# Kernel optimization log

Measured on AMD Instinct MI355X. Metric: run time of the kernel, lower is better.

## Reference

```python
import jax, jax.numpy as jnp
import numpy as np

N = 50000      # nodes
E = 1250000    # edges (avg degree 32)
D = 64         # in_channels == hidden_channels
L = 3          # num_layers
IMPROVED_FILL = 2.0  # GCNConv(improved=True) self-loop weight


def setup_inputs() -> dict:
    key = jax.random.key(0)
    ks = jax.random.split(key, 6)
    x = jax.random.normal(ks[0], (N, D), dtype=jnp.float32)
    edge_index = jax.random.randint(ks[1], (2, E), 0, N, dtype=jnp.int64)
    edge_weight = jax.random.uniform(ks[2], (E,), dtype=jnp.float32)
    Ws = jax.random.normal(ks[3], (L, D, D), dtype=jnp.float32) / np.sqrt(D).astype(np.float32)
    bs = jnp.zeros((L, D), dtype=jnp.float32)
    Wf = jax.random.normal(ks[4], (D, 1), dtype=jnp.float32) / np.sqrt(D).astype(np.float32)
    bf = jnp.zeros((1,), dtype=jnp.float32)
    return dict(x=x, edge_index=edge_index, edge_weight=edge_weight,
                Ws=Ws, bs=bs, Wf=Wf, bf=bf, prob=0)


def _gcn_norm(edge_index, edge_weight, n):
    # add self-loops with fill value 2.0 (improved=True)
    loop = jnp.arange(n, dtype=edge_index.dtype)
    row = jnp.concatenate([edge_index[0], loop])  # source nodes (x_j)
    col = jnp.concatenate([edge_index[1], loop])  # target nodes (aggregation)
    w = jnp.concatenate([edge_weight,
                         jnp.full((n,), IMPROVED_FILL, edge_weight.dtype)])
    deg = jax.ops.segment_sum(w, col, num_segments=n)
    dis = jnp.where(deg > 0, jax.lax.rsqrt(deg), 0.0)  # deg^{-1/2}, inf->0
    norm = dis[row] * w * dis[col]                      # [E+N]
    return row, col, norm


def reference(x, edge_index, edge_weight, Ws, bs, Wf, bf, prob):
    n = x.shape[0]
    # gcn_norm depends only on graph structure; compute once, reuse per layer
    row, col, norm = _gcn_norm(edge_index, edge_weight, n)
    for l in range(Ws.shape[0]):
        h = x @ Ws[l]                                  # [N, D] linear transform
        msg = h[row] * norm[:, None]                   # gather + per-edge scale
        agg = jax.ops.segment_sum(msg, col, num_segments=n)  # scatter-add
        x = jax.nn.relu(agg + bs[l])
    # F.dropout(x, p=prob) with prob=0 -> identity (inference)
    return x @ Wf + bf                                 # [N, 1]
```

## Files before the change

kernel.cpp:

```cpp
#include <hip/hip_runtime.h>
#include <hip/hip_bf16.h>

#define DCH 64
#define NB_CSR 256
#define MAXBINS 256

typedef __attribute__((ext_vector_type(8))) short bfrag;
typedef __attribute__((ext_vector_type(4))) float ffrag;

static __device__ __forceinline__ unsigned short f2bf(float f) {
    unsigned u = __float_as_uint(f);
    unsigned r = (u + 0x7fffu + ((u >> 16) & 1u)) >> 16;
    return (unsigned short)r;
}
static __device__ __forceinline__ float bf2f(unsigned short s) {
    return __uint_as_float(((unsigned)s) << 16);
}

__global__ __launch_bounds__(1024) void binc_k(const int* __restrict__ col,
                                               unsigned* __restrict__ blkcnt, int e) {
    __shared__ unsigned bins[MAXBINS];
    int B = blockIdx.x, tid = threadIdx.x;
    int chunk = (e + NB_CSR - 1) / NB_CSR;
    int beg = B * chunk, end = min(e, beg + chunk);
    if (tid < MAXBINS) bins[tid] = 0;
    __syncthreads();
    for (int i = beg + tid; i < end; i += 1024)
        atomicAdd(&bins[col[i] >> 8], 1u);
    __syncthreads();
    if (tid < MAXBINS) blkcnt[B * MAXBINS + tid] = bins[tid];
}

__global__ __launch_bounds__(64) void bincur1_k(const unsigned* __restrict__ blkcnt,
                                                unsigned* __restrict__ blkcur,
                                                unsigned* __restrict__ tot) {
    int j = blockIdx.x, lane = threadIdx.x;
    unsigned carry = 0;
#pragma unroll
    for (int c = 0; c < NB_CSR; c += 64) {
        unsigned v = blkcnt[(size_t)(c + lane) * MAXBINS + j];
        unsigned s = v;
#pragma unroll
        for (int off = 1; off < 64; off <<= 1) {
            unsigned t = __shfl_up(s, off);
            if (lane >= off) s += t;
        }
        blkcur[(size_t)(c + lane) * MAXBINS + j] = carry + s - v;
        carry += __shfl(s, 63);
    }
    if (lane == 0) tot[j] = carry;
}

__global__ __launch_bounds__(256) void bincur2_k(const unsigned* __restrict__ tot,
                                                 int* __restrict__ binbase,
                                                 int* __restrict__ ptr,
                                                 int nbins, int n, int e) {
    __shared__ int wtot[4];
    int tid = threadIdx.x, lane = tid & 63, w = tid >> 6;
    int v = (tid < nbins) ? (int)tot[tid] : 0;
    int s = v;
#pragma unroll
    for (int off = 1; off < 64; off <<= 1) {
        int t = __shfl_up(s, off);
        if (lane >= off) s += t;
    }
    if (lane == 63) wtot[w] = s;
    __syncthreads();
    if (tid == 0) {
        int r = 0;
#pragma unroll
        for (int k = 0; k < 4; ++k) { int t = wtot[k]; wtot[k] = r; r += t; }
    }
    __syncthreads();
    int excl = s - v + wtot[w];
    if (tid < nbins) binbase[tid] = excl;
    if (tid == 0) { binbase[nbins] = e; ptr[n] = e; }
}

__global__ __launch_bounds__(1024) void binfill_k(const int* __restrict__ row,
                                                  const int* __restrict__ col,
                                                  const float* __restrict__ ew,
                                                  const unsigned* __restrict__ blkcur,
                                                  const int* __restrict__ binbase,
                                                  uint2* __restrict__ rec, int e) {
    __shared__ unsigned cur[MAXBINS];
    int B = blockIdx.x, tid = threadIdx.x;
    int chunk = (e + NB_CSR - 1) / NB_CSR;
    int beg = B * chunk, end = min(e, beg + chunk);
    if (tid < MAXBINS) cur[tid] = blkcur[(size_t)B * MAXBINS + tid]
                                + (unsigned)binbase[tid];
    __syncthreads();
    for (int i = beg + tid; i < end; i += 1024) {
        int c = col[i];
        unsigned slot = atomicAdd(&cur[c >> 8], 1u);
        rec[slot] = make_uint2((unsigned)row[i] | ((unsigned)(c & 255) << 20),
                               __float_as_uint(ew[i]));
    }
}

__global__ __launch_bounds__(1024) void csr_k(const uint2* __restrict__ rec,
                                              const int* __restrict__ binbase,
                                              int* __restrict__ ptr,
                                              uint2* __restrict__ edg,
                                              float* __restrict__ dis, int n) {
    __shared__ unsigned ncnt[256];
    __shared__ unsigned nbase[256];
    __shared__ float degs[256];
    int b = blockIdx.x, tid = threadIdx.x;
    int beg = binbase[b], end = binbase[b + 1];
    int node0 = b << 8;
    int nn = min(256, n - node0);
    if (tid < 256) { ncnt[tid] = 0; degs[tid] = 0.f; }
    __syncthreads();
    for (int i = beg + tid; i < end; i += 1024) {
        uint2 r = rec[i];
        unsigned c8 = r.x >> 20;
        atomicAdd(&ncnt[c8], 1u);
        atomicAdd(&degs[c8], __uint_as_float(r.y));
    }
    __syncthreads();
    if (tid < 64) {
        unsigned carry = (unsigned)beg;
#pragma unroll
        for (int c = 0; c < 256; c += 64) {
            unsigned v = ncnt[c + tid];
            unsigned s = v;
#pragma unroll
            for (int off = 1; off < 64; off <<= 1) {
                unsigned t = __shfl_up(s, off);
                if (tid >= off) s += t;
            }
            nbase[c + tid] = carry + s - v;
            carry += __shfl(s, 63);
        }
    }
    __syncthreads();
    if (tid < nn) {
        ptr[node0 + tid] = (int)nbase[tid];
        dis[node0 + tid] = rsqrtf(degs[tid] + 2.0f);
    }
    if (tid < 256) ncnt[tid] = 0;
    __syncthreads();
    for (int i = beg + tid; i < end; i += 1024) {
        uint2 r = rec[i];
        unsigned c8 = r.x >> 20;
        unsigned pos = nbase[c8] + atomicAdd(&ncnt[c8], 1u);
        edg[pos] = make_uint2(r.x & 0xFFFFFu, r.y);
    }
}

__global__ __launch_bounds__(256) void normw_k(uint2* __restrict__ edg,
                                               const float* __restrict__ dis, int e) {
    int i = blockIdx.x * 256 + threadIdx.x;
    if (i >= e) return;
    uint2 ev = edg[i];
    ((unsigned*)edg)[2 * i + 1] =
        __float_as_uint(__uint_as_float(ev.y) * dis[ev.x]);
}

__global__ __launch_bounds__(256) void pack_k(const float* __restrict__ Ws,
                                              short* __restrict__ wpk, int L) {
    int ent = blockIdx.x * 256 + threadIdx.x;
    if (ent >= L * 512) return;
    int layer = ent >> 9;
    int r = ent & 511;
    int lane = r & 63;
    int st = r >> 6;
    int s = st >> 2, t = st & 3;
    int quad = lane >> 4;
    int ncol = t * 16 + (lane & 15);
    const float* W = Ws + (size_t)layer * DCH * DCH;
    union { short sh[8]; int4 v; } hi, lo;
#pragma unroll
    for (int j = 0; j < 8; ++j) {
        int k = s * 32 + quad * 8 + j;
        float w = W[k * DCH + ncol];
        unsigned short h = f2bf(w);
        hi.sh[j] = (short)h;
        lo.sh[j] = (short)f2bf(w - bf2f(h));
    }
    *(int4*)(wpk + ((size_t)(layer * 2 + 0) * 512 + r) * 8) = hi.v;
    *(int4*)(wpk + ((size_t)(layer * 2 + 1) * 512 + r) * 8) = lo.v;
}

__global__ __launch_bounds__(256) void gemm_k(const float* __restrict__ x,
                                              const short* __restrict__ wpk_layer,
                                              unsigned short* __restrict__ hb, int n_tiles) {
    __shared__ short Wl[2][512 * 8];
    {
        const int4* src = (const int4*)wpk_layer;
        int4* dst = (int4*)&Wl[0][0];
        for (int i = threadIdx.x; i < 1024; i += 256) dst[i] = src[i];
    }
    __syncthreads();
    int wave = threadIdx.x >> 6, lane = threadIdx.x & 63;
    int tile = blockIdx.x * 4 + wave;
    if (tile >= n_tiles) return;
    int m = lane & 15, quad = lane >> 4;
    int row = tile * 16 + m;

    float av[2][8];
    {
        const float4* p0 = (const float4*)(x + (size_t)row * DCH + quad * 8);
        const float4* p1 = (const float4*)(x + (size_t)row * DCH + 32 + quad * 8);
        float4 a0 = p0[0], a1 = p0[1], b0 = p1[0], b1 = p1[1];
        av[0][0] = a0.x; av[0][1] = a0.y; av[0][2] = a0.z; av[0][3] = a0.w;
        av[0][4] = a1.x; av[0][5] = a1.y; av[0][6] = a1.z; av[0][7] = a1.w;
        av[1][0] = b0.x; av[1][1] = b0.y; av[1][2] = b0.z; av[1][3] = b0.w;
        av[1][4] = b1.x; av[1][5] = b1.y; av[1][6] = b1.z; av[1][7] = b1.w;
    }
    bfrag ah[2], al[2];
#pragma unroll
    for (int s = 0; s < 2; ++s)
#pragma unroll
        for (int j = 0; j < 8; ++j) {
            unsigned short hbv = f2bf(av[s][j]);
            ah[s][j] = (short)hbv;
            al[s][j] = (short)f2bf(av[s][j] - bf2f(hbv));
        }

#pragma unroll
    for (int t = 0; t < 4; ++t) {
        ffrag acc = {0.f, 0.f, 0.f, 0.f};
#pragma unroll
        for (int s = 0; s < 2; ++s) {
            bfrag wh = *(bfrag*)&Wl[0][((s * 4 + t) * 64 + lane) * 8];
            bfrag wl = *(bfrag*)&Wl[1][((s * 4 + t) * 64 + lane) * 8];
            acc = __builtin_amdgcn_mfma_f32_16x16x32_bf16(ah[s], wh, acc, 0, 0, 0);
            acc = __builtin_amdgcn_mfma_f32_16x16x32_bf16(al[s], wh, acc, 0, 0, 0);
            acc = __builtin_amdgcn_mfma_f32_16x16x32_bf16(ah[s], wl, acc, 0, 0, 0);
        }
        int colc = t * 16 + m;
#pragma unroll
        for (int r = 0; r < 4; ++r)
            hb[(size_t)(tile * 16 + quad * 4 + r) * DCH + colc] = f2bf(acc[r]);
    }
}

static __device__ __forceinline__ void gather_node(int node, int lane, int pp, int eo,
                                                   float dis_c,
                                                   const int* __restrict__ ptr,
                                                   const uint2* __restrict__ edg,
                                                   const unsigned* __restrict__ hbf,
                                                   float a[4]) {
    a[0] = a[1] = a[2] = a[3] = 0.f;
    if (eo == 0) {
        uint2 sv = *(const uint2*)(hbf + (size_t)node * 32 + 2 * pp);
        float wsl = 2.0f * dis_c;
        a[0] = wsl * __uint_as_float(sv.x << 16);
        a[1] = wsl * __uint_as_float(sv.x & 0xffff0000u);
        a[2] = wsl * __uint_as_float(sv.y << 16);
        a[3] = wsl * __uint_as_float(sv.y & 0xffff0000u);
    }
    int beg = ptr[node], end = ptr[node + 1];
    for (int base = beg; base < end; base += 64) {
        int idx = base + lane;
        int rv = 0; float nv = 0.f;
        if (idx < end) {
            uint2 ev = edg[idx];
            rv = (int)ev.x;
            nv = __uint_as_float(ev.y);
        }
        int m = min(64, end - base);
        int steps = (((m + 3) >> 2) + 7) & ~7;
        for (int j0 = 0; j0 < steps; j0 += 8) {
            uint2 hv[8]; float nn[8];
#pragma unroll
            for (int q = 0; q < 8; ++q) {
                int eidx = 4 * (j0 + q) + eo;
                int r = __shfl(rv, eidx);
                nn[q] = __shfl(nv, eidx);
                hv[q] = *(const uint2*)(hbf + (size_t)r * 32 + 2 * pp);
            }
#pragma unroll
            for (int q = 0; q < 8; ++q) {
                a[0] += __uint_as_float(hv[q].x << 16) * nn[q];
                a[1] += __uint_as_float(hv[q].x & 0xffff0000u) * nn[q];
                a[2] += __uint_as_float(hv[q].y << 16) * nn[q];
                a[3] += __uint_as_float(hv[q].y & 0xffff0000u) * nn[q];
            }
        }
    }
#pragma unroll
    for (int j = 0; j < 4; ++j) {
        a[j] += __shfl_xor(a[j], 16);
        a[j] += __shfl_xor(a[j], 32);
    }
}

__global__ __launch_bounds__(256) void gg_k(const int* __restrict__ ptr,
                                            const uint2* __restrict__ edg,
                                            const float* __restrict__ dis,
                                            const unsigned* __restrict__ hbf,
                                            const float* __restrict__ b,
                                            const short* __restrict__ wpk_next,
                                            unsigned short* __restrict__ hb_out, int n) {
    __shared__ float xs[16][68];
    int w = threadIdx.x >> 6, lane = threadIdx.x & 63;
    int pp = lane & 15, eo = lane >> 4;
    int tile = blockIdx.x;
    float4 bv = ((const float4*)b)[pp];
#pragma unroll 1
    for (int i = 0; i < 4; ++i) {
        int node = tile * 16 + w * 4 + i;
        if (node < n) {
            float dis_c = dis[node];
            float a[4];
            gather_node(node, lane, pp, eo, dis_c, ptr, edg, hbf, a);
            if (eo == 0) {
                float4 o;
                o.x = fmaxf(dis_c * a[0] + bv.x, 0.f);
                o.y = fmaxf(dis_c * a[1] + bv.y, 0.f);
                o.z = fmaxf(dis_c * a[2] + bv.z, 0.f);
                o.w = fmaxf(dis_c * a[3] + bv.w, 0.f);
                *(float4*)&xs[w * 4 + i][4 * pp] = o;
            }
        }
    }
    __syncthreads();
    int m = lane & 15, quad = lane >> 4, t = w;
    bfrag ah[2], al[2];
#pragma unroll
    for (int s = 0; s < 2; ++s)
#pragma unroll
        for (int j = 0; j < 8; ++j) {
            float v = xs[m][s * 32 + quad * 8 + j];
            unsigned short hbv = f2bf(v);
            ah[s][j] = (short)hbv;
            al[s][j] = (short)f2bf(v - bf2f(hbv));
        }
    ffrag acc = {0.f, 0.f, 0.f, 0.f};
#pragma unroll
    for (int s = 0; s < 2; ++s) {
        bfrag wh = *(const bfrag*)(wpk_next + ((size_t)((s * 4 + t) * 64 + lane)) * 8);
        bfrag wl = *(const bfrag*)(wpk_next + ((size_t)(512 + (s * 4 + t) * 64 + lane)) * 8);
        acc = __builtin_amdgcn_mfma_f32_16x16x32_bf16(ah[s], wh, acc, 0, 0, 0);
        acc = __builtin_amdgcn_mfma_f32_16x16x32_bf16(al[s], wh, acc, 0, 0, 0);
        acc = __builtin_amdgcn_mfma_f32_16x16x32_bf16(ah[s], wl, acc, 0, 0, 0);
    }
    int colc = t * 16 + m;
#pragma unroll
    for (int r = 0; r < 4; ++r) {
        int orow = tile * 16 + quad * 4 + r;
        if (orow < n) hb_out[(size_t)orow * DCH + colc] = f2bf(acc[r]);
    }
}

__global__ __launch_bounds__(256) void gf_k(const int* __restrict__ ptr,
                                            const uint2* __restrict__ edg,
                                            const float* __restrict__ dis,
                                            const unsigned* __restrict__ hbf,
                                            const float* __restrict__ b,
                                            const float* __restrict__ Wf,
                                            const float* __restrict__ bf,
                                            float* __restrict__ out, int n) {
    int node = blockIdx.x * 4 + (threadIdx.x >> 6);
    int lane = threadIdx.x & 63;
    if (node >= n) return;
    int pp = lane & 15, eo = lane >> 4;
    float dis_c = dis[node];
    float a[4];
    gather_node(node, lane, pp, eo, dis_c, ptr, edg, hbf, a);
    float4 bv = ((const float4*)b)[pp];
    float4 wv = ((const float4*)Wf)[pp];
    float v = fmaxf(dis_c * a[0] + bv.x, 0.f) * wv.x
            + fmaxf(dis_c * a[1] + bv.y, 0.f) * wv.y
            + fmaxf(dis_c * a[2] + bv.z, 0.f) * wv.z
            + fmaxf(dis_c * a[3] + bv.w, 0.f) * wv.w;
#pragma unroll
    for (int off = 8; off > 0; off >>= 1) v += __shfl_xor(v, off);
    if (lane == 0) out[node] = v + bf[0];
}

extern "C" void kernel_launch(void* const* d_in, const int* in_sizes, int n_in,
                              void* d_out, int out_size, void* d_ws, size_t ws_size,
                              hipStream_t stream) {
    const float* x0 = (const float*)d_in[0];
    const int*   ei = (const int*)d_in[1];
    const float* ew = (const float*)d_in[2];
    const float* Ws = (const float*)d_in[3];
    const float* bs = (const float*)d_in[4];
    const float* Wf = (const float*)d_in[5];
    const float* bf = (const float*)d_in[6];

    const int n = in_sizes[0] / DCH;
    const int e = in_sizes[2];
    const int L = in_sizes[3] / (DCH * DCH);

    const int* row = ei;
    const int* col = ei + e;
    const int nbins = (n + 255) >> 8;

    size_t off = 0;
    auto alloc = [&](size_t bytes) {
        off = (off + 255) & ~(size_t)255;
        void* r = (char*)d_ws + off;
        off += bytes;
        return r;
    };
    int*      ptr     = (int*)     alloc((size_t)(n + 1) * 4);
    float*    dis     = (float*)   alloc((size_t)n * 4);
    short*    wpk     = (short*)   alloc((size_t)L * 2 * 512 * 8 * 2);
    uint2*    edg     = (uint2*)   alloc((size_t)e * 8);
    unsigned* blkcnt  = (unsigned*)alloc((size_t)NB_CSR * MAXBINS * 4);
    unsigned* blkcur  = (unsigned*)alloc((size_t)NB_CSR * MAXBINS * 4);
    unsigned* tot     = (unsigned*)alloc((size_t)MAXBINS * 4);
    int*      binbase = (int*)     alloc((size_t)(MAXBINS + 1) * 4);
    size_t szR = (size_t)e * 8;
    size_t szH = (size_t)2 * n * DCH * 2;
    unsigned char* regA = (unsigned char*)alloc(szR > szH ? szR : szH);
    uint2* rec = (uint2*)regA;
    unsigned short* hb_a = (unsigned short*)regA;
    unsigned short* hb_b = hb_a + (size_t)n * DCH;

    dim3 blk(256);
    const int n_tiles = (n + 15) / 16;

    binc_k   <<<dim3(NB_CSR), dim3(1024), 0, stream>>>(col, blkcnt, e);
    bincur1_k<<<dim3(nbins), dim3(64), 0, stream>>>(blkcnt, blkcur, tot);
    bincur2_k<<<dim3(1), blk, 0, stream>>>(tot, binbase, ptr, nbins, n, e);
    binfill_k<<<dim3(NB_CSR), dim3(1024), 0, stream>>>(row, col, ew, blkcur, binbase, rec, e);
    csr_k    <<<dim3(nbins), dim3(1024), 0, stream>>>(rec, binbase, ptr, edg, dis, n);
    normw_k  <<<dim3((e + 255) / 256), blk, 0, stream>>>(edg, dis, e);
    pack_k   <<<dim3((L * 512 + 255) / 256), blk, 0, stream>>>(Ws, wpk, L);

    const size_t wstride = (size_t)2 * 512 * 8;
    gemm_k<<<dim3((n_tiles + 3) / 4), blk, 0, stream>>>(x0, wpk, hb_a, n_tiles);
    gg_k  <<<dim3(n_tiles), blk, 0, stream>>>(ptr, edg, dis, (const unsigned*)hb_a,
                                              bs, wpk + wstride, hb_b, n);
    gg_k  <<<dim3(n_tiles), blk, 0, stream>>>(ptr, edg, dis, (const unsigned*)hb_b,
                                              bs + DCH, wpk + 2 * wstride, hb_a, n);
    gf_k  <<<dim3((n + 3) / 4), blk, 0, stream>>>(ptr, edg, dis, (const unsigned*)hb_a,
                                                  bs + 2 * DCH, Wf, bf, (float*)d_out, n);
}
```

Measured before the change: 209.0 us.

## Assign one 16-lane group per node in GCN gather instead of one wavefront

Rewrites the neighbor gather so each 16-lane quarter-wave handles a whole node and walks its edges serially, reading edge records directly instead of spreading edges across the wavefront and broadcasting them with shuffles. This drops the cross-lane shuffle reductions and the per-wave serial loop over four nodes, and lets a wave process four nodes at once. The final-layer kernel now packs 16 nodes per block. The cost is load imbalance from uneven degrees within a wave, and each lane group issues its edge-record loads independently, so those loads are no longer coalesced.

Measured after the change: 235.6 us. 1.13x slower.

```diff
diff --git a/kernel.cpp b/kernel.cpp
--- a/kernel.cpp
+++ b/kernel.cpp
@@ -15,6 +15,12 @@
 }
 static __device__ __forceinline__ float bf2f(unsigned short s) {
     return __uint_as_float(((unsigned)s) << 16);
+}
+static __device__ __forceinline__ float bf_lo(unsigned u) {
+    return __uint_as_float(u << 16);
+}
+static __device__ __forceinline__ float bf_hi(unsigned u) {
+    return __uint_as_float(u & 0xffff0000u);
 }
 
 __global__ __launch_bounds__(1024) void binc_k(const int* __restrict__ col,
@@ -237,54 +243,38 @@
     }
 }
 
-static __device__ __forceinline__ void gather_node(int node, int lane, int pp, int eo,
-                                                   float dis_c,
-                                                   const int* __restrict__ ptr,
-                                                   const uint2* __restrict__ edg,
-                                                   const unsigned* __restrict__ hbf,
-                                                   float a[4]) {
-    a[0] = a[1] = a[2] = a[3] = 0.f;
-    if (eo == 0) {
-        uint2 sv = *(const uint2*)(hbf + (size_t)node * 32 + 2 * pp);
-        float wsl = 2.0f * dis_c;
-        a[0] = wsl * __uint_as_float(sv.x << 16);
-        a[1] = wsl * __uint_as_float(sv.x & 0xffff0000u);
-        a[2] = wsl * __uint_as_float(sv.y << 16);
-        a[3] = wsl * __uint_as_float(sv.y & 0xffff0000u);
-    }
+static __device__ __forceinline__ void gather_node16(int node, int pp,
+                                                     float dis_c,
+                                                     const int* __restrict__ ptr,
+                                                     const uint2* __restrict__ edg,
+                                                     const unsigned* __restrict__ hbf,
+                                                     float a[4]) {
     int beg = ptr[node], end = ptr[node + 1];
-    for (int base = beg; base < end; base += 64) {
-        int idx = base + lane;
-        int rv = 0; float nv = 0.f;
-        if (idx < end) {
-            uint2 ev = edg[idx];
-            rv = (int)ev.x;
-            nv = __uint_as_float(ev.y);
-        }
-        int m = min(64, end - base);
-        int steps = (((m + 3) >> 2) + 7) & ~7;
-        for (int j0 = 0; j0 < steps; j0 += 8) {
-            uint2 hv[8]; float nn[8];
-#pragma unroll
-            for (int q = 0; q < 8; ++q) {
-                int eidx = 4 * (j0 + q) + eo;
-                int r = __shfl(rv, eidx);
-                nn[q] = __shfl(nv, eidx);
-                hv[q] = *(const uint2*)(hbf + (size_t)r * 32 + 2 * pp);
-            }
-#pragma unroll
-            for (int q = 0; q < 8; ++q) {
-                a[0] += __uint_as_float(hv[q].x << 16) * nn[q];
-                a[1] += __uint_as_float(hv[q].x & 0xffff0000u) * nn[q];
-                a[2] += __uint_as_float(hv[q].y << 16) * nn[q];
-                a[3] += __uint_as_float(hv[q].y & 0xffff0000u) * nn[q];
-            }
-        }
-    }
-#pragma unroll
-    for (int j = 0; j < 4; ++j) {
-        a[j] += __shfl_xor(a[j], 16);
-        a[j] += __shfl_xor(a[j], 32);
+    uint2 sv = *(const uint2*)(hbf + (size_t)node * 32 + 2 * pp);
+    float wsl = 2.0f * dis_c;
+    a[0] = wsl * bf_lo(sv.x);
+    a[1] = wsl * bf_hi(sv.x);
+    a[2] = wsl * bf_lo(sv.y);
+    a[3] = wsl * bf_hi(sv.y);
+    for (int j0 = beg; j0 < end; j0 += 8) {
+        uint2 rr[8];
+#pragma unroll
+        for (int q = 0; q < 8; ++q) {
+            int e = j0 + q;
+            rr[q] = (e < end) ? edg[e] : make_uint2(0u, 0u);
+        }
+        uint2 hv[8];
+#pragma unroll
+        for (int q = 0; q < 8; ++q)
+            hv[q] = *(const uint2*)(hbf + (size_t)rr[q].x * 32 + 2 * pp);
+#pragma unroll
+        for (int q = 0; q < 8; ++q) {
+            float nn = __uint_as_float(rr[q].y);
+            a[0] += bf_lo(hv[q].x) * nn;
+            a[1] += bf_hi(hv[q].x) * nn;
+            a[2] += bf_lo(hv[q].y) * nn;
+            a[3] += bf_hi(hv[q].y) * nn;
+        }
     }
 }
 
@@ -297,25 +287,21 @@
                                             unsigned short* __restrict__ hb_out, int n) {
     __shared__ float xs[16][68];
     int w = threadIdx.x >> 6, lane = threadIdx.x & 63;
-    int pp = lane & 15, eo = lane >> 4;
+    int pp = lane & 15, sub = lane >> 4;
+    int slot = w * 4 + sub;
     int tile = blockIdx.x;
-    float4 bv = ((const float4*)b)[pp];
-#pragma unroll 1
-    for (int i = 0; i < 4; ++i) {
-        int node = tile * 16 + w * 4 + i;
-        if (node < n) {
-            float dis_c = dis[node];
-            float a[4];
-            gather_node(node, lane, pp, eo, dis_c, ptr, edg, hbf, a);
-            if (eo == 0) {
-                float4 o;
-                o.x = fmaxf(dis_c * a[0] + bv.x, 0.f);
-                o.y = fmaxf(dis_c * a[1] + bv.y, 0.f);
-                o.z = fmaxf(dis_c * a[2] + bv.z, 0.f);
-                o.w = fmaxf(dis_c * a[3] + bv.w, 0.f);
-                *(float4*)&xs[w * 4 + i][4 * pp] = o;
-            }
-        }
+    int node = tile * 16 + slot;
+    if (node < n) {
+        float dis_c = dis[node];
+        float a[4];
+        gather_node16(node, pp, dis_c, ptr, edg, hbf, a);
+        float4 bv = ((const float4*)b)[pp];
+        float4 o;
+        o.x = fmaxf(dis_c * a[0] + bv.x, 0.f);
+        o.y = fmaxf(dis_c * a[1] + bv.y, 0.f);
+        o.z = fmaxf(dis_c * a[2] + bv.z, 0.f);
+        o.w = fmaxf(dis_c * a[3] + bv.w, 0.f);
+        *(float4*)&xs[slot][4 * pp] = o;
     }
     __syncthreads();
     int m = lane & 15, quad = lane >> 4, t = w;
@@ -354,13 +340,14 @@
                                             const float* __restrict__ Wf,
                                             const float* __restrict__ bf,
                                             float* __restrict__ out, int n) {
-    int node = blockIdx.x * 4 + (threadIdx.x >> 6);
     int lane = threadIdx.x & 63;
+    int pp = lane & 15, sub = lane >> 4;
+    int slot = (threadIdx.x >> 6) * 4 + sub;
+    int node = blockIdx.x * 16 + slot;
     if (node >= n) return;
-    int pp = lane & 15, eo = lane >> 4;
     float dis_c = dis[node];
     float a[4];
-    gather_node(node, lane, pp, eo, dis_c, ptr, edg, hbf, a);
+    gather_node16(node, pp, dis_c, ptr, edg, hbf, a);
     float4 bv = ((const float4*)b)[pp];
     float4 wv = ((const float4*)Wf)[pp];
     float v = fmaxf(dis_c * a[0] + bv.x, 0.f) * wv.x
@@ -369,7 +356,7 @@
             + fmaxf(dis_c * a[3] + bv.w, 0.f) * wv.w;
 #pragma unroll
     for (int off = 8; off > 0; off >>= 1) v += __shfl_xor(v, off);
-    if (lane == 0) out[node] = v + bf[0];
+    if (pp == 0) out[node] = v + bf[0];
 }
 
 extern "C" void kernel_launch(void* const* d_in, const int* in_sizes, int n_in,
@@ -430,6 +417,6 @@
                                               bs, wpk + wstride, hb_b, n);
     gg_k  <<<dim3(n_tiles), blk, 0, stream>>>(ptr, edg, dis, (const unsigned*)hb_b,
                                               bs + DCH, wpk + 2 * wstride, hb_a, n);
-    gf_k  <<<dim3((n + 3) / 4), blk, 0, stream>>>(ptr, edg, dis, (const unsigned*)hb_a,
-                                                  bs + 2 * DCH, Wf, bf, (float*)d_out, n);
-}
+    gf_k  <<<dim3((n + 15) / 16), blk, 0, stream>>>(ptr, edg, dis, (const unsigned*)hb_a,
+                                                    bs + 2 * DCH, Wf, bf, (float*)d_out, n);
+}
```

## Fuse CSR build into one persistent kernel with grid barriers; prefetch edges in gg_k

Applied to the files above, without the earlier changes.

The seven preprocessing launches (bin count, two scans, bin fill, CSR build, norm weighting, weight packing) are merged into one 256-block persistent kernel that uses atomic grid-wide barriers between phases. The norm weighting is folded into the final CSR scatter. This removes launch gaps and one full pass over the edge array. In the gather-GEMM kernel, the node pointers are now staged in shared memory and the next node's edge records are prefetched, so edge loads overlap with the current node's gather. The grid barrier assumes all 256 blocks of 1024 threads are co-resident, and it deadlocks if they are not.

After: 341.8 us. 1.64x slower.

```diff
diff --git a/kernel.cpp b/kernel.cpp
--- a/kernel.cpp
+++ b/kernel.cpp
@@ -4,6 +4,7 @@
 #define DCH 64
 #define NB_CSR 256
 #define MAXBINS 256
+#define NBLK 256
 
 typedef __attribute__((ext_vector_type(8))) short bfrag;
 typedef __attribute__((ext_vector_type(4))) float ffrag;
@@ -16,171 +17,186 @@
 static __device__ __forceinline__ float bf2f(unsigned short s) {
     return __uint_as_float(((unsigned)s) << 16);
 }
-
-__global__ __launch_bounds__(1024) void binc_k(const int* __restrict__ col,
-                                               unsigned* __restrict__ blkcnt, int e) {
-    __shared__ unsigned bins[MAXBINS];
-    int B = blockIdx.x, tid = threadIdx.x;
-    int chunk = (e + NB_CSR - 1) / NB_CSR;
-    int beg = B * chunk, end = min(e, beg + chunk);
-    if (tid < MAXBINS) bins[tid] = 0;
+static __device__ __forceinline__ float bf_lo(unsigned u) {
+    return __uint_as_float(u << 16);
+}
+static __device__ __forceinline__ float bf_hi(unsigned u) {
+    return __uint_as_float(u & 0xffff0000u);
+}
+
+static __device__ __forceinline__ void gbar(unsigned* bar, int idx) {
     __syncthreads();
-    for (int i = beg + tid; i < end; i += 1024)
-        atomicAdd(&bins[col[i] >> 8], 1u);
+    if (threadIdx.x == 0) {
+        __threadfence();
+        __hip_atomic_fetch_add(bar + idx, 1u, __ATOMIC_ACQ_REL,
+                               __HIP_MEMORY_SCOPE_AGENT);
+        while (__hip_atomic_load(bar + idx, __ATOMIC_ACQUIRE,
+                                 __HIP_MEMORY_SCOPE_AGENT) < (unsigned)NBLK)
+            __builtin_amdgcn_s_sleep(2);
+        __threadfence();
+    }
     __syncthreads();
-    if (tid < MAXBINS) blkcnt[B * MAXBINS + tid] = bins[tid];
-}
-
-__global__ __launch_bounds__(64) void bincur1_k(const unsigned* __restrict__ blkcnt,
-                                                unsigned* __restrict__ blkcur,
-                                                unsigned* __restrict__ tot) {
-    int j = blockIdx.x, lane = threadIdx.x;
-    unsigned carry = 0;
-#pragma unroll
-    for (int c = 0; c < NB_CSR; c += 64) {
-        unsigned v = blkcnt[(size_t)(c + lane) * MAXBINS + j];
-        unsigned s = v;
-#pragma unroll
-        for (int off = 1; off < 64; off <<= 1) {
-            unsigned t = __shfl_up(s, off);
-            if (lane >= off) s += t;
-        }
-        blkcur[(size_t)(c + lane) * MAXBINS + j] = carry + s - v;
-        carry += __shfl(s, 63);
-    }
-    if (lane == 0) tot[j] = carry;
-}
-
-__global__ __launch_bounds__(256) void bincur2_k(const unsigned* __restrict__ tot,
-                                                 int* __restrict__ binbase,
-                                                 int* __restrict__ ptr,
-                                                 int nbins, int n, int e) {
-    __shared__ int wtot[4];
-    int tid = threadIdx.x, lane = tid & 63, w = tid >> 6;
-    int v = (tid < nbins) ? (int)tot[tid] : 0;
-    int s = v;
-#pragma unroll
-    for (int off = 1; off < 64; off <<= 1) {
-        int t = __shfl_up(s, off);
-        if (lane >= off) s += t;
-    }
-    if (lane == 63) wtot[w] = s;
-    __syncthreads();
-    if (tid == 0) {
-        int r = 0;
-#pragma unroll
-        for (int k = 0; k < 4; ++k) { int t = wtot[k]; wtot[k] = r; r += t; }
-    }
-    __syncthreads();
-    int excl = s - v + wtot[w];
-    if (tid < nbins) binbase[tid] = excl;
-    if (tid == 0) { binbase[nbins] = e; ptr[n] = e; }
-}
-
-__global__ __launch_bounds__(1024) void binfill_k(const int* __restrict__ row,
-                                                  const int* __restrict__ col,
-                                                  const float* __restrict__ ew,
-                                                  const unsigned* __restrict__ blkcur,
-                                                  const int* __restrict__ binbase,
-                                                  uint2* __restrict__ rec, int e) {
-    __shared__ unsigned cur[MAXBINS];
-    int B = blockIdx.x, tid = threadIdx.x;
-    int chunk = (e + NB_CSR - 1) / NB_CSR;
-    int beg = B * chunk, end = min(e, beg + chunk);
-    if (tid < MAXBINS) cur[tid] = blkcur[(size_t)B * MAXBINS + tid]
-                                + (unsigned)binbase[tid];
-    __syncthreads();
-    for (int i = beg + tid; i < end; i += 1024) {
-        int c = col[i];
-        unsigned slot = atomicAdd(&cur[c >> 8], 1u);
-        rec[slot] = make_uint2((unsigned)row[i] | ((unsigned)(c & 255) << 20),
-                               __float_as_uint(ew[i]));
-    }
-}
-
-__global__ __launch_bounds__(1024) void csr_k(const uint2* __restrict__ rec,
-                                              const int* __restrict__ binbase,
-                                              int* __restrict__ ptr,
-                                              uint2* __restrict__ edg,
-                                              float* __restrict__ dis, int n) {
-    __shared__ unsigned ncnt[256];
-    __shared__ unsigned nbase[256];
-    __shared__ float degs[256];
-    int b = blockIdx.x, tid = threadIdx.x;
-    int beg = binbase[b], end = binbase[b + 1];
-    int node0 = b << 8;
-    int nn = min(256, n - node0);
-    if (tid < 256) { ncnt[tid] = 0; degs[tid] = 0.f; }
-    __syncthreads();
-    for (int i = beg + tid; i < end; i += 1024) {
-        uint2 r = rec[i];
-        unsigned c8 = r.x >> 20;
-        atomicAdd(&ncnt[c8], 1u);
-        atomicAdd(&degs[c8], __uint_as_float(r.y));
-    }
-    __syncthreads();
-    if (tid < 64) {
-        unsigned carry = (unsigned)beg;
-#pragma unroll
-        for (int c = 0; c < 256; c += 64) {
-            unsigned v = ncnt[c + tid];
+}
+
+__global__ __launch_bounds__(1024) void prep_k(const int* __restrict__ row,
+                                               const int* __restrict__ col,
+                                               const float* __restrict__ ew,
+                                               const float* __restrict__ Ws,
+                                               unsigned* __restrict__ blkcnt,
+                                               unsigned* __restrict__ blkcur,
+                                               unsigned* __restrict__ tot,
+                                               int* __restrict__ binbase,
+                                               int* __restrict__ ptr,
+                                               float* __restrict__ dis,
+                                               uint2* __restrict__ rec,
+                                               uint2* __restrict__ edg,
+                                               short* __restrict__ wpk,
+                                               unsigned* __restrict__ bar,
+                                               int n, int e, int L, int nbins) {
+    __shared__ unsigned sA[256];
+    __shared__ unsigned sB[256];
+    __shared__ float    sC[256];
+    const int B = blockIdx.x, tid = threadIdx.x;
+    const int chunk = (e + NB_CSR - 1) / NB_CSR;
+
+    {
+        int beg = B * chunk, end = min(e, beg + chunk);
+        if (tid < 256) sA[tid] = 0;
+        __syncthreads();
+        for (int i = beg + tid; i < end; i += 1024)
+            atomicAdd(&sA[col[i] >> 8], 1u);
+        __syncthreads();
+        if (tid < 256) blkcnt[B * 256 + tid] = sA[tid];
+    }
+    gbar(bar, 0);
+
+    if (B < nbins && tid < 64) {
+        int j = B, lane = tid;
+        unsigned carry = 0;
+#pragma unroll
+        for (int c = 0; c < NB_CSR; c += 64) {
+            unsigned v = blkcnt[(size_t)(c + lane) * 256 + j];
             unsigned s = v;
 #pragma unroll
             for (int off = 1; off < 64; off <<= 1) {
                 unsigned t = __shfl_up(s, off);
-                if (tid >= off) s += t;
-            }
-            nbase[c + tid] = carry + s - v;
+                if (lane >= off) s += t;
+            }
+            blkcur[(size_t)(c + lane) * 256 + j] = carry + s - v;
             carry += __shfl(s, 63);
         }
-    }
-    __syncthreads();
-    if (tid < nn) {
-        ptr[node0 + tid] = (int)nbase[tid];
-        dis[node0 + tid] = rsqrtf(degs[tid] + 2.0f);
-    }
-    if (tid < 256) ncnt[tid] = 0;
-    __syncthreads();
-    for (int i = beg + tid; i < end; i += 1024) {
-        uint2 r = rec[i];
-        unsigned c8 = r.x >> 20;
-        unsigned pos = nbase[c8] + atomicAdd(&ncnt[c8], 1u);
-        edg[pos] = make_uint2(r.x & 0xFFFFFu, r.y);
-    }
-}
-
-__global__ __launch_bounds__(256) void normw_k(uint2* __restrict__ edg,
-                                               const float* __restrict__ dis, int e) {
-    int i = blockIdx.x * 256 + threadIdx.x;
-    if (i >= e) return;
-    uint2 ev = edg[i];
-    ((unsigned*)edg)[2 * i + 1] =
-        __float_as_uint(__uint_as_float(ev.y) * dis[ev.x]);
-}
-
-__global__ __launch_bounds__(256) void pack_k(const float* __restrict__ Ws,
-                                              short* __restrict__ wpk, int L) {
-    int ent = blockIdx.x * 256 + threadIdx.x;
-    if (ent >= L * 512) return;
-    int layer = ent >> 9;
-    int r = ent & 511;
-    int lane = r & 63;
-    int st = r >> 6;
-    int s = st >> 2, t = st & 3;
-    int quad = lane >> 4;
-    int ncol = t * 16 + (lane & 15);
-    const float* W = Ws + (size_t)layer * DCH * DCH;
-    union { short sh[8]; int4 v; } hi, lo;
-#pragma unroll
-    for (int j = 0; j < 8; ++j) {
-        int k = s * 32 + quad * 8 + j;
-        float w = W[k * DCH + ncol];
-        unsigned short h = f2bf(w);
-        hi.sh[j] = (short)h;
-        lo.sh[j] = (short)f2bf(w - bf2f(h));
-    }
-    *(int4*)(wpk + ((size_t)(layer * 2 + 0) * 512 + r) * 8) = hi.v;
-    *(int4*)(wpk + ((size_t)(layer * 2 + 1) * 512 + r) * 8) = lo.v;
+        if (lane == 0) tot[j] = carry;
+    }
+    if (B == 255) {
+        for (int ent = tid; ent < L * 512; ent += 1024) {
+            int layer = ent >> 9;
+            int r = ent & 511;
+            int lane = r & 63;
+            int st = r >> 6;
+            int s = st >> 2, t = st & 3;
+            int quad = lane >> 4;
+            int ncol = t * 16 + (lane & 15);
+            const float* W = Ws + (size_t)layer * DCH * DCH;
+            union { short sh[8]; int4 v; } hi, lo;
+#pragma unroll
+            for (int j = 0; j < 8; ++j) {
+                int k = s * 32 + quad * 8 + j;
+                float w = W[k * DCH + ncol];
+                unsigned short h = f2bf(w);
+                hi.sh[j] = (short)h;
+                lo.sh[j] = (short)f2bf(w - bf2f(h));
+            }
+            *(int4*)(wpk + ((size_t)(layer * 2 + 0) * 512 + r) * 8) = hi.v;
+            *(int4*)(wpk + ((size_t)(layer * 2 + 1) * 512 + r) * 8) = lo.v;
+        }
+    }
+    gbar(bar, 1);
+
+    if (B == 0) {
+        int lane = tid & 63, wv = tid >> 6;
+        int v = (tid < nbins) ? (int)tot[tid] : 0;
+        int s = v;
+#pragma unroll
+        for (int off = 1; off < 64; off <<= 1) {
+            int t = __shfl_up(s, off);
+            if (lane >= off) s += t;
+        }
+        if (lane == 63) ((int*)sB)[wv] = s;
+        __syncthreads();
+        if (tid == 0) {
+            int r = 0;
+#pragma unroll
+            for (int k = 0; k < 16; ++k) { int t = ((int*)sB)[k]; ((int*)sB)[k] = r; r += t; }
+        }
+        __syncthreads();
+        int excl = s - v + ((int*)sB)[wv];
+        if (tid < nbins) binbase[tid] = excl;
+        if (tid == 0) { binbase[nbins] = e; ptr[n] = e; }
+    }
+    gbar(bar, 2);
+
+    {
+        int beg = B * chunk, end = min(e, beg + chunk);
+        if (tid < 256) sA[tid] = blkcur[(size_t)B * 256 + tid]
+                               + (unsigned)binbase[tid];
+        __syncthreads();
+        for (int i = beg + tid; i < end; i += 1024) {
+            int c = col[i];
+            unsigned slot = atomicAdd(&sA[c >> 8], 1u);
+            rec[slot] = make_uint2((unsigned)row[i] | ((unsigned)(c & 255) << 20),
+                                   __float_as_uint(ew[i]));
+        }
+    }
+    gbar(bar, 3);
+
+    int ebeg = 0, eend = 0;
+    const int node0 = B << 8;
+    if (B < nbins) {
+        ebeg = binbase[B]; eend = binbase[B + 1];
+        int nn = min(256, n - node0);
+        if (tid < 256) { sA[tid] = 0; sC[tid] = 0.f; }
+        __syncthreads();
+        for (int i = ebeg + tid; i < eend; i += 1024) {
+            uint2 r = rec[i];
+            unsigned c8 = r.x >> 20;
+            atomicAdd(&sA[c8], 1u);
+            atomicAdd(&sC[c8], __uint_as_float(r.y));
+        }
+        __syncthreads();
+        if (tid < 64) {
+            unsigned carry = (unsigned)ebeg;
+#pragma unroll
+            for (int c = 0; c < 256; c += 64) {
+                unsigned v = sA[c + tid];
+                unsigned s = v;
+#pragma unroll
+                for (int off = 1; off < 64; off <<= 1) {
+                    unsigned t = __shfl_up(s, off);
+                    if (tid >= off) s += t;
+                }
+                sB[c + tid] = carry + s - v;
+                carry += __shfl(s, 63);
+            }
+        }
+        __syncthreads();
+        if (tid < nn) {
+            ptr[node0 + tid] = (int)sB[tid];
+            dis[node0 + tid] = rsqrtf(sC[tid] + 2.0f);
+        }
+        if (tid < 256) sA[tid] = 0;
+    }
+    gbar(bar, 4);
+
+    if (B < nbins) {
+        for (int i = ebeg + tid; i < eend; i += 1024) {
+            uint2 r = rec[i];
+            unsigned c8 = r.x >> 20;
+            unsigned src = r.x & 0xFFFFFu;
+            unsigned pos = sB[c8] + atomicAdd(&sA[c8], 1u);
+            edg[pos] = make_uint2(src,
+                __float_as_uint(__uint_as_float(r.y) * dis[src]));
+        }
+    }
 }
 
 __global__ __launch_bounds__(256) void gemm_k(const float* __restrict__ x,
@@ -247,10 +263,10 @@
     if (eo == 0) {
         uint2 sv = *(const uint2*)(hbf + (size_t)node * 32 + 2 * pp);
         float wsl = 2.0f * dis_c;
-        a[0] = wsl * __uint_as_float(sv.x << 16);
-        a[1] = wsl * __uint_as_float(sv.x & 0xffff0000u);
-        a[2] = wsl * __uint_as_float(sv.y << 16);
-        a[3] = wsl * __uint_as_float(sv.y & 0xffff0000u);
+        a[0] = wsl * bf_lo(sv.x);
+        a[1] = wsl * bf_hi(sv.x);
+        a[2] = wsl * bf_lo(sv.y);
+        a[3] = wsl * bf_hi(sv.y);
     }
     int beg = ptr[node], end = ptr[node + 1];
     for (int base = beg; base < end; base += 64) {
@@ -274,10 +290,10 @@
             }
 #pragma unroll
             for (int q = 0; q < 8; ++q) {
-                a[0] += __uint_as_float(hv[q].x << 16) * nn[q];
-                a[1] += __uint_as_float(hv[q].x & 0xffff0000u) * nn[q];
-                a[2] += __uint_as_float(hv[q].y << 16) * nn[q];
-                a[3] += __uint_as_float(hv[q].y & 0xffff0000u) * nn[q];
+                a[0] += bf_lo(hv[q].x) * nn[q];
+                a[1] += bf_hi(hv[q].x) * nn[q];
+                a[2] += bf_lo(hv[q].y) * nn[q];
+                a[3] += bf_hi(hv[q].y) * nn[q];
             }
         }
     }
@@ -296,25 +312,80 @@
                                             const short* __restrict__ wpk_next,
                                             unsigned short* __restrict__ hb_out, int n) {
     __shared__ float xs[16][68];
+    __shared__ int pt[17];
     int w = threadIdx.x >> 6, lane = threadIdx.x & 63;
     int pp = lane & 15, eo = lane >> 4;
     int tile = blockIdx.x;
+    if (threadIdx.x < 17)
+        pt[threadIdx.x] = ptr[min(tile * 16 + (int)threadIdx.x, n)];
+    __syncthreads();
     float4 bv = ((const float4*)b)[pp];
+    int s0 = w * 4;
+    uint2 evp;
+    {
+        int beg = pt[s0], end = pt[s0 + 1];
+        int idx = beg + lane;
+        evp = (idx < end) ? edg[idx] : make_uint2(0u, 0u);
+    }
 #pragma unroll 1
     for (int i = 0; i < 4; ++i) {
-        int node = tile * 16 + w * 4 + i;
-        if (node < n) {
-            float dis_c = dis[node];
-            float a[4];
-            gather_node(node, lane, pp, eo, dis_c, ptr, edg, hbf, a);
-            if (eo == 0) {
-                float4 o;
-                o.x = fmaxf(dis_c * a[0] + bv.x, 0.f);
-                o.y = fmaxf(dis_c * a[1] + bv.y, 0.f);
-                o.z = fmaxf(dis_c * a[2] + bv.z, 0.f);
-                o.w = fmaxf(dis_c * a[3] + bv.w, 0.f);
-                *(float4*)&xs[w * 4 + i][4 * pp] = o;
-            }
+        int slot = s0 + i;
+        int node = tile * 16 + slot;
+        int beg = pt[slot], end = pt[slot + 1];
+        uint2 ev0 = evp;
+        if (i < 3) {
+            int b2 = pt[slot + 1], e2 = pt[slot + 2];
+            int idx = b2 + lane;
+            evp = (idx < e2) ? edg[idx] : make_uint2(0u, 0u);
+        }
+        if (node >= n) continue;
+        float dis_c = dis[node];
+        float a0 = 0.f, a1 = 0.f, a2 = 0.f, a3 = 0.f;
+        if (eo == 0) {
+            uint2 sv = *(const uint2*)(hbf + (size_t)node * 32 + 2 * pp);
+            float wsl = 2.0f * dis_c;
+            a0 = wsl * bf_lo(sv.x); a1 = wsl * bf_hi(sv.x);
+            a2 = wsl * bf_lo(sv.y); a3 = wsl * bf_hi(sv.y);
+        }
+        for (int base = beg; base < end; base += 64) {
+            int rv; float nv;
+            if (base == beg) {
+                rv = (int)ev0.x; nv = __uint_as_float(ev0.y);
+            } else {
+                int idx = base + lane;
+                uint2 ev = (idx < end) ? edg[idx] : make_uint2(0u, 0u);
+                rv = (int)ev.x; nv = __uint_as_float(ev.y);
+            }
+            int m = min(64, end - base);
+            int steps = (((m + 3) >> 2) + 7) & ~7;
+            for (int j0 = 0; j0 < steps; j0 += 8) {
+                uint2 hv[8]; float nn[8];
+#pragma unroll
+                for (int q = 0; q < 8; ++q) {
+                    int eidx = 4 * (j0 + q) + eo;
+                    int r = __shfl(rv, eidx);
+                    nn[q] = __shfl(nv, eidx);
+                    hv[q] = *(const uint2*)(hbf + (size_t)r * 32 + 2 * pp);
+                }
+#pragma unroll
+                for (int q = 0; q < 8; ++q) {
+                    float ww = nn[q];
+                    a0 += bf_lo(hv[q].x) * ww; a1 += bf_hi(hv[q].x) * ww;
+                    a2 += bf_lo(hv[q].y) * ww; a3 += bf_hi(hv[q].y) * ww;
+                }
+            }
+        }
+        a0 += __shfl_xor(a0, 16); a0 += __shfl_xor(a0, 32);
+        a1 += __shfl_xor(a1, 16); a1 += __shfl_xor(a1, 32);
+        a2 += __shfl_xor(a2, 16); a2 += __shfl_xor(a2, 32);
+        a3 += __shfl_xor(a3, 16); a3 += __shfl_xor(a3, 32);
+        if (eo == 0) {
+            float4 o;
+            o.x = fmaxf(dis_c * a0 + bv.x, 0.f);
+            o.y = fmaxf(dis_c * a1 + bv.y, 0.f);
+            o.z = fmaxf(dis_c * a2 + bv.z, 0.f);
+            o.w = fmaxf(dis_c * a3 + bv.w, 0.f);
+            *(float4*)&xs[slot][4 * pp] = o;
         }
     }
     __syncthreads();
@@ -398,6 +469,7 @@
         off += bytes;
         return r;
     };
+    unsigned* bar     = (unsigned*)alloc(64);
     int*      ptr     = (int*)     alloc((size_t)(n + 1) * 4);
     float*    dis     = (float*)   alloc((size_t)n * 4);
     short*    wpk     = (short*)   alloc((size_t)L * 2 * 512 * 8 * 2);
@@ -416,13 +488,11 @@
     dim3 blk(256);
     const int n_tiles = (n + 15) / 16;
 
-    binc_k   <<<dim3(NB_CSR), dim3(1024), 0, stream>>>(col, blkcnt, e);
-    bincur1_k<<<dim3(nbins), dim3(64), 0, stream>>>(blkcnt, blkcur, tot);
-    bincur2_k<<<dim3(1), blk, 0, stream>>>(tot, binbase, ptr, nbins, n, e);
-    binfill_k<<<dim3(NB_CSR), dim3(1024), 0, stream>>>(row, col, ew, blkcur, binbase, rec, e);
-    csr_k    <<<dim3(nbins), dim3(1024), 0, stream>>>(rec, binbase, ptr, edg, dis, n);
-    normw_k  <<<dim3((e + 255) / 256), blk, 0, stream>>>(edg, dis, e);
-    pack_k   <<<dim3((L * 512 + 255) / 256), blk, 0, stream>>>(Ws, wpk, L);
+    hipMemsetAsync(bar, 0, 64, stream);
+    prep_k<<<dim3(NBLK), dim3(1024), 0, stream>>>(row, col, ew, Ws,
+                                                  blkcnt, blkcur, tot, binbase,
+                                                  ptr, dis, rec, edg, wpk, bar,
+                                                  n, e, L, nbins);
 
     const size_t wstride = (size_t)2 * 512 * 8;
     gemm_k<<<dim3((n_tiles + 3) / 4), blk, 0, stream>>>(x0, wpk, hb_a, n_tiles);
```

## Split aggregation into feature-half passes and unfuse the next-layer GEMM

Applied to the files above, without the earlier changes.

Replaces the fused gather+GEMM kernel with an aggregation kernel that handles half of the 64 channels per launch. Eight lanes cover 32 channels, so each wave processes eight edges at once and the per-pass gathered working set is halved, which should improve L2 locality on random row gathers. The result is written as fp32 to a scratch buffer, then a separate gemm_k and a final dot kernel run. Edge-list loads are nontemporal. The cost is twice as many passes over the edge list, an extra fp32 round trip through memory, and more kernel launches.

New measurement: 305.6 us. +46.2%, slower.

```diff
diff --git a/kernel.cpp b/kernel.cpp
--- a/kernel.cpp
+++ b/kernel.cpp
@@ -15,6 +15,12 @@
 }
 static __device__ __forceinline__ float bf2f(unsigned short s) {
     return __uint_as_float(((unsigned)s) << 16);
+}
+static __device__ __forceinline__ float bf_lo(unsigned u) {
+    return __uint_as_float(u << 16);
+}
+static __device__ __forceinline__ float bf_hi(unsigned u) {
+    return __uint_as_float(u & 0xffff0000u);
 }
 
 __global__ __launch_bounds__(1024) void binc_k(const int* __restrict__ col,
@@ -237,139 +243,99 @@
     }
 }
 
-static __device__ __forceinline__ void gather_node(int node, int lane, int pp, int eo,
-                                                   float dis_c,
-                                                   const int* __restrict__ ptr,
-                                                   const uint2* __restrict__ edg,
-                                                   const unsigned* __restrict__ hbf,
-                                                   float a[4]) {
-    a[0] = a[1] = a[2] = a[3] = 0.f;
-    if (eo == 0) {
-        uint2 sv = *(const uint2*)(hbf + (size_t)node * 32 + 2 * pp);
-        float wsl = 2.0f * dis_c;
-        a[0] = wsl * __uint_as_float(sv.x << 16);
-        a[1] = wsl * __uint_as_float(sv.x & 0xffff0000u);
-        a[2] = wsl * __uint_as_float(sv.y << 16);
-        a[3] = wsl * __uint_as_float(sv.y & 0xffff0000u);
-    }
-    int beg = ptr[node], end = ptr[node + 1];
-    for (int base = beg; base < end; base += 64) {
-        int idx = base + lane;
-        int rv = 0; float nv = 0.f;
-        if (idx < end) {
-            uint2 ev = edg[idx];
-            rv = (int)ev.x;
-            nv = __uint_as_float(ev.y);
-        }
-        int m = min(64, end - base);
-        int steps = (((m + 3) >> 2) + 7) & ~7;
-        for (int j0 = 0; j0 < steps; j0 += 8) {
-            uint2 hv[8]; float nn[8];
-#pragma unroll
-            for (int q = 0; q < 8; ++q) {
-                int eidx = 4 * (j0 + q) + eo;
-                int r = __shfl(rv, eidx);
-                nn[q] = __shfl(nv, eidx);
-                hv[q] = *(const uint2*)(hbf + (size_t)r * 32 + 2 * pp);
-            }
-#pragma unroll
-            for (int q = 0; q < 8; ++q) {
-                a[0] += __uint_as_float(hv[q].x << 16) * nn[q];
-                a[1] += __uint_as_float(hv[q].x & 0xffff0000u) * nn[q];
-                a[2] += __uint_as_float(hv[q].y << 16) * nn[q];
-                a[3] += __uint_as_float(hv[q].y & 0xffff0000u) * nn[q];
-            }
-        }
-    }
-#pragma unroll
-    for (int j = 0; j < 4; ++j) {
-        a[j] += __shfl_xor(a[j], 16);
-        a[j] += __shfl_xor(a[j], 32);
-    }
-}
-
-__global__ __launch_bounds__(256) void gg_k(const int* __restrict__ ptr,
-                                            const uint2* __restrict__ edg,
-                                            const float* __restrict__ dis,
-                                            const unsigned* __restrict__ hbf,
-                                            const float* __restrict__ b,
-                                            const short* __restrict__ wpk_next,
-                                            unsigned short* __restrict__ hb_out, int n) {
-    __shared__ float xs[16][68];
+__global__ __launch_bounds__(256) void aggh_k(const int* __restrict__ ptr,
+                                              const uint2* __restrict__ edg,
+                                              const float* __restrict__ dis,
+                                              const unsigned* __restrict__ hbf,
+                                              const float* __restrict__ b,
+                                              float* __restrict__ X,
+                                              int n, int half) {
     int w = threadIdx.x >> 6, lane = threadIdx.x & 63;
-    int pp = lane & 15, eo = lane >> 4;
-    int tile = blockIdx.x;
-    float4 bv = ((const float4*)b)[pp];
+    int eo = lane >> 3, pp = lane & 7;
+    const unsigned* hb2 = hbf + half * 16 + 2 * pp;
 #pragma unroll 1
     for (int i = 0; i < 4; ++i) {
-        int node = tile * 16 + w * 4 + i;
-        if (node < n) {
-            float dis_c = dis[node];
-            float a[4];
-            gather_node(node, lane, pp, eo, dis_c, ptr, edg, hbf, a);
-            if (eo == 0) {
-                float4 o;
-                o.x = fmaxf(dis_c * a[0] + bv.x, 0.f);
-                o.y = fmaxf(dis_c * a[1] + bv.y, 0.f);
-                o.z = fmaxf(dis_c * a[2] + bv.z, 0.f);
-                o.w = fmaxf(dis_c * a[3] + bv.w, 0.f);
-                *(float4*)&xs[w * 4 + i][4 * pp] = o;
+        int node = blockIdx.x * 16 + w * 4 + i;
+        if (node >= n) continue;
+        float dc = dis[node];
+        float a0 = 0.f, a1 = 0.f, a2 = 0.f, a3 = 0.f;
+        if (eo == 0) {
+            uint2 sv = *(const uint2*)(hb2 + (size_t)node * 32);
+            float wsl = 2.0f * dc;
+            a0 = wsl * bf_lo(sv.x); a1 = wsl * bf_hi(sv.x);
+            a2 = wsl * bf_lo(sv.y); a3 = wsl * bf_hi(sv.y);
+        }
+        int beg = ptr[node], end = ptr[node + 1];
+        for (int base = beg; base < end; base += 64) {
+            int idx = base + lane;
+            int rv = 0; float nv = 0.f;
+            if (idx < end) {
+                unsigned long long ev = __builtin_nontemporal_load(
+                    (const unsigned long long*)&edg[idx]);
+                rv = (int)(unsigned)ev;
+                nv = __uint_as_float((unsigned)(ev >> 32));
             }
-        }
-    }
-    __syncthreads();
-    int m = lane & 15, quad = lane >> 4, t = w;
-    bfrag ah[2], al[2];
-#pragma unroll
-    for (int s = 0; s < 2; ++s)
-#pragma unroll
-        for (int j = 0; j < 8; ++j) {
-            float v = xs[m][s * 32 + quad * 8 + j];
-            unsigned short hbv = f2bf(v);
-            ah[s][j] = (short)hbv;
-            al[s][j] = (short)f2bf(v - bf2f(hbv));
-        }
-    ffrag acc = {0.f, 0.f, 0.f, 0.f};
-#pragma unroll
-    for (int s = 0; s < 2; ++s) {
-        bfrag wh = *(const bfrag*)(wpk_next + ((size_t)((s * 4 + t) * 64 + lane)) * 8);
-        bfrag wl = *(const bfrag*)(wpk_next + ((size_t)(512 + (s * 4 + t) * 64 + lane)) * 8);
-        acc = __builtin_amdgcn_mfma_f32_16x16x32_bf16(ah[s], wh, acc, 0, 0, 0);
-        acc = __builtin_amdgcn_mfma_f32_16x16x32_bf16(al[s], wh, acc, 0, 0, 0);
-        acc = __builtin_amdgcn_mfma_f32_16x16x32_bf16(ah[s], wl, acc, 0, 0, 0);
-    }
-    int colc = t * 16 + m;
-#pragma unroll
-    for (int r = 0; r < 4; ++r) {
-        int orow = tile * 16 + quad * 4 + r;
-        if (orow < n) hb_out[(size_t)orow * DCH + colc] = f2bf(acc[r]);
-    }
-}
-
-__global__ __launch_bounds__(256) void gf_k(const int* __restrict__ ptr,
-                                            const uint2* __restrict__ edg,
-                                            const float* __restrict__ dis,
-                                            const unsigned* __restrict__ hbf,
-                                            const float* __restrict__ b,
-                                            const float* __restrict__ Wf,
-                                            const float* __restrict__ bf,
-                                            float* __restrict__ out, int n) {
+            int m = min(64, end - base);
+            if (m <= 32) {
+                uint2 hv[4]; float nn[4];
+#pragma unroll
+                for (int q = 0; q < 4; ++q) {
+                    int eidx = 8 * q + eo;
+                    int r = __shfl(rv, eidx);
+                    nn[q] = __shfl(nv, eidx);
+                    hv[q] = *(const uint2*)(hb2 + (size_t)r * 32);
+                }
+#pragma unroll
+                for (int q = 0; q < 4; ++q) {
+                    float ww = nn[q];
+                    a0 += bf_lo(hv[q].x) * ww; a1 += bf_hi(hv[q].x) * ww;
+                    a2 += bf_lo(hv[q].y) * ww; a3 += bf_hi(hv[q].y) * ww;
+                }
+            } else {
+                uint2 hv[8]; float nn[8];
+#pragma unroll
+                for (int q = 0; q < 8; ++q) {
+                    int eidx = 8 * q + eo;
+                    int r = __shfl(rv, eidx);
+                    nn[q] = __shfl(nv, eidx);
+                    hv[q] = *(const uint2*)(hb2 + (size_t)r * 32);
+                }
+#pragma unroll
+                for (int q = 0; q < 8; ++q) {
+                    float ww = nn[q];
+                    a0 += bf_lo(hv[q].x) * ww; a1 += bf_hi(hv[q].x) * ww;
+                    a2 += bf_lo(hv[q].y) * ww; a3 += bf_hi(hv[q].y) * ww;
+                }
+            }
+        }
+        a0 += __shfl_xor(a0, 8); a0 += __shfl_xor(a0, 16); a0 += __shfl_xor(a0, 32);
+        a1 += __shfl_xor(a1, 8); a1 += __shfl_xor(a1, 16); a1 += __shfl_xor(a1, 32);
+        a2 += __shfl_xor(a2, 8); a2 += __shfl_xor(a2, 16); a2 += __shfl_xor(a2, 32);
+        a3 += __shfl_xor(a3, 8); a3 += __shfl_xor(a3, 16); a3 += __shfl_xor(a3, 32);
+        if (eo == 0) {
+            float4 bv = *(const float4*)(b + half * 32 + 4 * pp);
+            ffrag o;
+            o[0] = fmaxf(dc * a0 + bv.x, 0.f);
+            o[1] = fmaxf(dc * a1 + bv.y, 0.f);
+            o[2] = fmaxf(dc * a2 + bv.z, 0.f);
+            o[3] = fmaxf(dc * a3 + bv.w, 0.f);
+            __builtin_nontemporal_store(o,
+                (ffrag*)(X + (size_t)node * DCH + half * 32 + 4 * pp));
+        }
+    }
+}
+
+__global__ __launch_bounds__(256) void dot_k(const float* __restrict__ X,
+                                             const float* __restrict__ Wf,
+                                             const float* __restrict__ bfs,
+                                             float* __restrict__ out, int n) {
     int node = blockIdx.x * 4 + (threadIdx.x >> 6);
     int lane = threadIdx.x & 63;
     if (node >= n) return;
-    int pp = lane & 15, eo = lane >> 4;
-    float dis_c = dis[node];
-    float a[4];
-    gather_node(node, lane, pp, eo, dis_c, ptr, edg, hbf, a);
-    float4 bv = ((const float4*)b)[pp];
-    float4 wv = ((const float4*)Wf)[pp];
-    float v = fmaxf(dis_c * a[0] + bv.x, 0.f) * wv.x
-            + fmaxf(dis_c * a[1] + bv.y, 0.f) * wv.y
-            + fmaxf(dis_c * a[2] + bv.z, 0.f) * wv.z
-            + fmaxf(dis_c * a[3] + bv.w, 0.f) * wv.w;
-#pragma unroll
-    for (int off = 8; off > 0; off >>= 1) v += __shfl_xor(v, off);
-    if (lane == 0) out[node] = v + bf[0];
+    float v = X[(size_t)node * DCH + lane] * Wf[lane];
+#pragma unroll
+    for (int off = 32; off > 0; off >>= 1) v += __shfl_xor(v, off);
+    if (lane == 0) out[node] = v + bfs[0];
 }
 
 extern "C" void kernel_launch(void* const* d_in, const int* in_sizes, int n_in,
@@ -407,14 +373,16 @@
     unsigned* tot     = (unsigned*)alloc((size_t)MAXBINS * 4);
     int*      binbase = (int*)     alloc((size_t)(MAXBINS + 1) * 4);
     size_t szR = (size_t)e * 8;
-    size_t szH = (size_t)2 * n * DCH * 2;
-    unsigned char* regA = (unsigned char*)alloc(szR > szH ? szR : szH);
+    size_t szX = (size_t)n * DCH * 4;
+    unsigned char* regA = (unsigned char*)alloc(szR > szX ? szR : szX);
     uint2* rec = (uint2*)regA;
-    unsigned short* hb_a = (unsigned short*)regA;
+    float* Xf  = (float*)regA;
+    unsigned short* hb_a = (unsigned short*)alloc((size_t)2 * n * DCH * 2);
     unsigned short* hb_b = hb_a + (size_t)n * DCH;
 
     dim3 blk(256);
     const int n_tiles = (n + 15) / 16;
+    const int n_nblk  = (n + 15) / 16;
 
     binc_k   <<<dim3(NB_CSR), dim3(1024), 0, stream>>>(col, blkcnt, e);
     bincur1_k<<<dim3(nbins), dim3(64), 0, stream>>>(blkcnt, blkcur, tot);
@@ -426,10 +394,22 @@
 
     const size_t wstride = (size_t)2 * 512 * 8;
     gemm_k<<<dim3((n_tiles + 3) / 4), blk, 0, stream>>>(x0, wpk, hb_a, n_tiles);
-    gg_k  <<<dim3(n_tiles), blk, 0, stream>>>(ptr, edg, dis, (const unsigned*)hb_a,
-                                              bs, wpk + wstride, hb_b, n);
-    gg_k  <<<dim3(n_tiles), blk, 0, stream>>>(ptr, edg, dis, (const unsigned*)hb_b,
-                                              bs + DCH, wpk + 2 * wstride, hb_a, n);
-    gf_k  <<<dim3((n + 3) / 4), blk, 0, stream>>>(ptr, edg, dis, (const unsigned*)hb_a,
-                                                  bs + 2 * DCH, Wf, bf, (float*)d_out, n);
-}
+
+    aggh_k<<<dim3(n_nblk), blk, 0, stream>>>(ptr, edg, dis, (const unsigned*)hb_a,
+                                             bs, Xf, n, 0);
+    aggh_k<<<dim3(n_nblk), blk, 0, stream>>>(ptr, edg, dis, (const unsigned*)hb_a,
+                                             bs, Xf, n, 1);
+    gemm_k<<<dim3((n_tiles + 3) / 4), blk, 0, stream>>>(Xf, wpk + wstride, hb_b, n_tiles);
+
+    aggh_k<<<dim3(n_nblk), blk, 0, stream>>>(ptr, edg, dis, (const unsigned*)hb_b,
+                                             bs + DCH, Xf, n, 0);
+    aggh_k<<<dim3(n_nblk), blk, 0, stream>>>(ptr, edg, dis, (const unsigned*)hb_b,
+                                             bs + DCH, Xf, n, 1);
+    gemm_k<<<dim3((n_tiles + 3) / 4), blk, 0, stream>>>(Xf, wpk + 2 * wstride, hb_a, n_tiles);
+
+    aggh_k<<<dim3(n_nblk), blk, 0, stream>>>(ptr, edg, dis, (const unsigned*)hb_a,
+                                             bs + 2 * DCH, Xf, n, 0);
+    aggh_k<<<dim3(n_nblk), blk, 0, stream>>>(ptr, edg, dis, (const unsigned*)hb_a,
+                                             bs + 2 * DCH, Xf, n, 1);
+    dot_k <<<dim3((n + 3) / 4), blk, 0, stream>>>(Xf, Wf, bf, (float*)d_out, n);
+}
```
